# Kernel tuning notes

Measured on AMD Instinct MI355X. Metric: run time of the kernel, lower is better.

Reference implementation:

```python
import jax, jax.numpy as jnp
import numpy as np
from jax import lax

B, C, H, W = 4, 192, 64, 64
D_STATE, D_CONV, EXPAND = 16, 4, 2
D_INNER = EXPAND * C           # 384
DT_RANK = (C + 15) // 16       # 12 (mamba_ssm default ceil(d_model/16))


def setup_inputs() -> dict:
    key = jax.random.key(0)
    ks = jax.random.split(key, 12)
    sc = lambda k, shape, s=0.02: (jax.random.normal(k, shape, jnp.float32) * s)
    x = jax.random.normal(ks[0], (B, C, H, W), jnp.float32)
    norm_w = jnp.ones((C,), jnp.float32)
    norm_b = jnp.zeros((C,), jnp.float32)
    in_proj_w = sc(ks[1], (2 * D_INNER, C))
    conv_w = sc(ks[2], (D_INNER, D_CONV), 0.1)
    conv_b = jnp.zeros((D_INNER,), jnp.float32)
    x_proj_w = sc(ks[3], (DT_RANK + 2 * D_STATE, D_INNER))
    dt_proj_w = sc(ks[4], (D_INNER, DT_RANK), 0.1)
    # dt bias init so softplus(dt_bias) is in a realistic [1e-3, 1e-1] range
    dt0 = jax.random.uniform(ks[5], (D_INNER,), jnp.float32, 0.001, 0.1)
    dt_proj_b = jnp.log(jnp.expm1(dt0))
    A_log = jnp.log(jnp.broadcast_to(
        jnp.arange(1, D_STATE + 1, dtype=jnp.float32), (D_INNER, D_STATE)))
    D = jnp.ones((D_INNER,), jnp.float32)
    out_proj_w = sc(ks[6], (C, D_INNER))
    return {"x": x, "norm_w": norm_w, "norm_b": norm_b, "in_proj_w": in_proj_w,
            "conv_w": conv_w, "conv_b": conv_b, "x_proj_w": x_proj_w,
            "dt_proj_w": dt_proj_w, "dt_proj_b": dt_proj_b, "A_log": A_log,
            "D": D, "out_proj_w": out_proj_w}


def _mamba2d(x, norm_w, norm_b, in_proj_w, conv_w, conv_b, x_proj_w,
             dt_proj_w, dt_proj_b, A_log, D, out_proj_w):
    b, c, h, w = x.shape
    L = h * w
    seq = x.reshape(b, c, L).transpose(0, 2, 1)            # (B, L, C)
    # LayerNorm over channel dim
    mu = seq.mean(-1, keepdims=True)
    var = ((seq - mu) ** 2).mean(-1, keepdims=True)
    seqn = (seq - mu) * lax.rsqrt(var + 1e-5) * norm_w + norm_b
    # in_proj -> (x, z)
    xz = seqn @ in_proj_w.T                                # (B, L, 2*d_inner)
    xin, z = jnp.split(xz, 2, axis=-1)
    # causal depthwise conv1d over L
    xc = xin.transpose(0, 2, 1)                            # (B, d_inner, L)
    xc = lax.conv_general_dilated(xc, conv_w[:, None, :], (1,),
                                  [(D_CONV - 1, 0)],
                                  feature_group_count=D_INNER)
    xc = jax.nn.silu(xc + conv_b[None, :, None])
    xs = xc.transpose(0, 2, 1)                             # (B, L, d_inner)
    # input-dependent dt, B, C
    dbl = xs @ x_proj_w.T                                  # (B, L, dt_rank+2n)
    dt = dbl[..., :DT_RANK]
    Bm = dbl[..., DT_RANK:DT_RANK + D_STATE]               # (B, L, n)
    Cm = dbl[..., DT_RANK + D_STATE:]                      # (B, L, n)
    dt = jax.nn.softplus(dt @ dt_proj_w.T + dt_proj_b)     # (B, L, d_inner)
    A = -jnp.exp(A_log)                                    # (d_inner, n)
    dA = jnp.exp(dt[..., None] * A)                        # (B, L, d_inner, n)
    dBx = jnp.einsum('bld,bln->bldn', dt * xs, Bm)         # (B, L, d_inner, n)
    # selective scan over L
    def step(hcar, inp):
        dA_t, dBx_t, C_t = inp
        hcar = dA_t * hcar + dBx_t                         # (B, d_inner, n)
        y_t = jnp.einsum('bdn,bn->bd', hcar, C_t)
        return hcar, y_t
    h0 = jnp.zeros((b, D_INNER, D_STATE), xs.dtype)
    _, ys = lax.scan(step, h0, (jnp.moveaxis(dA, 1, 0),
                                jnp.moveaxis(dBx, 1, 0),
                                jnp.moveaxis(Cm, 1, 0)))
    y = jnp.moveaxis(ys, 0, 1) + xs * D                    # (B, L, d_inner)
    y = y * jax.nn.silu(z)
    out = y @ out_proj_w.T                                 # (B, L, C)
    return x + out.transpose(0, 2, 1).reshape(b, c, h, w)


def reference(x, norm_w, norm_b, in_proj_w, conv_w, conv_b, x_proj_w,
              dt_proj_w, dt_proj_b, A_log, D, out_proj_w):
    return _mamba2d(x, norm_w, norm_b, in_proj_w, conv_w, conv_b, x_proj_w,
                    dt_proj_w, dt_proj_b, A_log, D, out_proj_w)
```

## Files before the change

kernel.cpp:

```cpp
#include <hip/hip_runtime.h>
#include <hip/hip_bf16.h>

constexpr int B_ = 4;
constexpr int C_ = 192;
constexpr int L_ = 4096;
constexpr int DI = 384;
constexpr int DSs = 16;
constexpr int DTR = 12;
constexpr int NDBL = 44;
constexpr int NCHUNK = 256;
constexpr int CSZ = 16;
constexpr int NSUP = 16;

constexpr size_t BL = (size_t)B_ * L_;

constexpr size_t F_SEQN = 0;
constexpr size_t F_XIN  = F_SEQN + BL * C_ / 2;
constexpr size_t F_Z    = F_XIN + BL * DI / 2;
constexpr size_t F_XSB  = F_Z + BL * DI / 2;
constexpr size_t F_DBL  = F_XSB + BL * DI / 2;
constexpr size_t F_DT   = F_DBL + BL * NDBL;
constexpr size_t F_SBUF = F_DT + BL * DI / 2;
constexpr size_t F_HLOC = F_SBUF + (size_t)B_ * NCHUNK * DI;
constexpr size_t F_SPRE = F_HLOC + (size_t)B_ * NCHUNK * DI * 16 / 2;
constexpr size_t F_HSUP = F_SPRE + (size_t)B_ * NCHUNK * DI;
constexpr size_t F_SSUP = F_HSUP + (size_t)B_ * NSUP * 16 * DI;
constexpr size_t F_ISUP = F_SSUP + (size_t)B_ * NSUP * DI;
constexpr size_t F_WBUF = F_ISUP + (size_t)B_ * NSUP * 16 * DI;

typedef __attribute__((ext_vector_type(8))) short bf16x8;
typedef __attribute__((ext_vector_type(4))) float f32x4;

__device__ __forceinline__ unsigned short f2bf(float v) {
  unsigned x = __builtin_bit_cast(unsigned, v);
  unsigned r = x + 0x7FFFu + ((x >> 16) & 1u);
  return (unsigned short)(r >> 16);
}
__device__ __forceinline__ float bf2f(unsigned short u) {
  return __builtin_bit_cast(float, (unsigned)u << 16);
}
__device__ __forceinline__ void gload16(const void* g, void* l) {
  __builtin_amdgcn_global_load_lds((const __attribute__((address_space(1))) void*)g,
                                   (__attribute__((address_space(3))) void*)l, 16, 0, 0);
}
#define MFMA16(a, b, c) __builtin_amdgcn_mfma_f32_16x16x32_bf16(a, b, c, 0, 0, 0)

__global__ __launch_bounds__(256) void k_ln(const float* __restrict__ x,
                                            const float* __restrict__ nw,
                                            const float* __restrict__ nb,
                                            unsigned short* __restrict__ seqn,
                                            const float* __restrict__ ipw,
                                            const float* __restrict__ xpw,
                                            const float* __restrict__ opw,
                                            unsigned short* __restrict__ wbuf) {
  if (blockIdx.x >= 1024) {
    int t = (blockIdx.x - 1024) * 256 + threadIdx.x;
    if (t < 239616) {
      float v;
      if (t < 147456) v = ipw[t];
      else if (t < 165888) {
        int j = t - 147456;
        int r = j / 384, c = j - r * 384;
        v = (r < 44) ? xpw[r * 384 + c] : 0.f;
      } else v = opw[t - 165888];
      wbuf[t] = f2bf(v);
    }
    return;
  }
  __shared__ unsigned short xt[192][18];
  __shared__ float ps[16][16], ps2[16][16];
  __shared__ float mu_[16], rs_[16];
  __shared__ float wsh[192], bsh[192];
  int tid = threadIdx.x;
  int blk = blockIdx.x;
  int b = blk >> 8;
  int l0 = (blk & 255) << 4;
  const float* xb = x + (size_t)b * C_ * L_;
  for (int idx = tid; idx < 192 * 4; idx += 256) {
    int c = idx >> 2, lq = idx & 3;
    float4 v = *(const float4*)&xb[(size_t)c * L_ + l0 + (lq << 2)];
    ushort2 u0, u1;
    u0.x = f2bf(v.x); u0.y = f2bf(v.y);
    u1.x = f2bf(v.z); u1.y = f2bf(v.w);
    *(ushort2*)&xt[c][(lq << 2)] = u0;
    *(ushort2*)&xt[c][(lq << 2) + 2] = u1;
  }
  if (tid < 192) { wsh[tid] = nw[tid]; bsh[tid] = nb[tid]; }
  __syncthreads();
  int ll = tid & 15, q = tid >> 4;
  float s = 0.f, ss = 0.f;
  for (int c = q * 12; c < q * 12 + 12; ++c) {
    float v = bf2f(xt[c][ll]);
    s += v; ss += v * v;
  }
  ps[q][ll] = s; ps2[q][ll] = ss;
  __syncthreads();
  if (q == 0) {
    float st = 0.f, sst = 0.f;
#pragma unroll
    for (int g = 0; g < 16; ++g) { st += ps[g][ll]; sst += ps2[g][ll]; }
    float mu = st * (1.f / 192.f);
    float var = sst * (1.f / 192.f) - mu * mu;
    mu_[ll] = mu; rs_[ll] = rsqrtf(var + 1e-5f);
  }
  __syncthreads();
  unsigned short* so = seqn + ((size_t)b * L_ + l0) * C_;
  for (int idx = tid; idx < 16 * 192; idx += 256) {
    int l = idx / 192, c = idx - l * 192;
    so[idx] = f2bf((bf2f(xt[c][l]) - mu_[l]) * rs_[l] * wsh[c] + bsh[c]);
  }
}

__global__ __launch_bounds__(256) void k_inproj(const unsigned short* __restrict__ A,
                                                const unsigned short* __restrict__ W,
                                                unsigned short* __restrict__ xin,
                                                unsigned short* __restrict__ z) {
  __shared__ unsigned short smem[16384];
  unsigned short* As = smem;
  unsigned short* Bs = smem + 8192;
  int tid = threadIdx.x;
  int w = tid >> 6, l = tid & 63;
  int wr = w >> 1, wc = w & 1;
  int m0 = blockIdx.x << 7;
  int n0 = blockIdx.y << 7;
  f32x4 acc[4][4];
#pragma unroll
  for (int i = 0; i < 4; ++i)
#pragma unroll
    for (int j = 0; j < 4; ++j) acc[i][j] = (f32x4){0.f, 0.f, 0.f, 0.f};
  int lr = l & 15, lk = l >> 4;
  for (int kt = 0; kt < 3; ++kt) {
    int k0 = kt * 64;
    if (kt) __syncthreads();
#pragma unroll
    for (int i = 0; i < 4; ++i) {
      int row = (i << 5) + (tid >> 3);
      int gc = k0 + (((tid & 7) ^ (row & 7)) << 3);
      gload16(A + (size_t)(m0 + row) * 192 + gc, &As[(i << 11) + (w << 9)]);
      gload16(W + (size_t)(n0 + row) * 192 + gc, &Bs[(i << 11) + (w << 9)]);
    }
    __syncthreads();
#pragma unroll
    for (int ks = 0; ks < 2; ++ks) {
      int s = (ks << 2) + lk;
      bf16x8 af[4], bfr[4];
#pragma unroll
      for (int mi = 0; mi < 4; ++mi) {
        int r = (wr << 6) + (mi << 4) + lr;
        af[mi] = *(const bf16x8*)&As[r * 64 + ((s ^ (r & 7)) << 3)];
      }
#pragma unroll
      for (int ni = 0; ni < 4; ++ni) {
        int r = (wc << 6) + (ni << 4) + lr;
        bfr[ni] = *(const bf16x8*)&Bs[r * 64 + ((s ^ (r & 7)) << 3)];
      }
#pragma unroll
      for (int mi = 0; mi < 4; ++mi)
#pragma unroll
        for (int ni = 0; ni < 4; ++ni) acc[mi][ni] = MFMA16(af[mi], bfr[ni], acc[mi][ni]);
    }
  }
  __syncthreads();
#pragma unroll
  for (int mi = 0; mi < 4; ++mi)
#pragma unroll
    for (int ni = 0; ni < 4; ++ni) {
      int col = (wc << 6) + (ni << 4) + lr;
#pragma unroll
      for (int r = 0; r < 4; ++r) {
        int row = (wr << 6) + (mi << 4) + (lk << 2) + r;
        smem[(row << 7) + col] = f2bf(acc[mi][ni][r]);
      }
    }
  __syncthreads();
#pragma unroll
  for (int i = 0; i < 8; ++i) {
    int chunk = i * 256 + tid;
    int row = chunk >> 4, cq = chunk & 15;
    int n = n0 + (cq << 3);
    unsigned short* dst = (n < 384) ? (xin + (size_t)(m0 + row) * DI + n)
                                    : (z + (size_t)(m0 + row) * DI + (n - 384));
    *(bf16x8*)dst = *(const bf16x8*)&smem[(row << 7) + (cq << 3)];
  }
}

__global__ __launch_bounds__(384) void k_convx(const unsigned short* __restrict__ xin,
                                               const float* __restrict__ cw,
                                               const float* __restrict__ cb,
                                               const unsigned short* __restrict__ W,
                                               unsigned short* __restrict__ xsb,
                                               float* __restrict__ dbl) {
  __shared__ unsigned short xs[6 * 2048];
  __shared__ unsigned short Bs[3072];
  int tid = threadIdx.x;
  int w = tid >> 6, l = tid & 63;
  int b = blockIdx.y;
  int l0 = blockIdx.x << 5;
  int d = tid;
  float4 w4 = *(const float4*)&cw[d * 4];
  float bb = cb[d];
  const unsigned short* xp = xin + ((size_t)b * L_ + l0) * DI + d;
  unsigned short* op = xsb + ((size_t)b * L_ + l0) * DI + d;
  float x0 = 0.f, x1 = 0.f, x2 = 0.f;
  if (l0 > 0) {
    x0 = bf2f(*(xp - 3 * DI));
    x1 = bf2f(*(xp - 2 * DI));
    x2 = bf2f(*(xp - DI));
  }
  int kt = d >> 6, col = d & 63, g = col >> 3, e = col & 7;
  unsigned short* xsrow = xs + kt * 2048;
  for (int r = 0; r < 32; ++r) {
    float xv = bf2f(xp[(size_t)r * DI]);
    float a = bb + w4.x * x0 + w4.y * x1 + w4.z * x2 + w4.w * xv;
    float sv = a * __builtin_amdgcn_rcpf(1.f + __expf(-a));
    unsigned short sb = f2bf(sv);
    xsrow[r * 64 + ((g ^ (r & 7)) << 3) + e] = sb;
    op[(size_t)r * DI] = sb;
    x0 = x1; x1 = x2; x2 = xv;
  }
  __syncthreads();
  int lr = l & 15, lk = l >> 4;
  f32x4 acc[3];
#pragma unroll
  for (int i = 0; i < 3; ++i) acc[i] = (f32x4){0.f, 0.f, 0.f, 0.f};
  for (int kt2 = 0; kt2 < 6; ++kt2) {
    int k0 = kt2 * 64;
    if (kt2) __syncthreads();
    {
      int row = tid >> 3;
      int gc = k0 + (((tid & 7) ^ (row & 7)) << 3);
      gload16(W + (size_t)row * 384 + gc, &Bs[w << 9]);
    }
    __syncthreads();
    if (w < 2) {
#pragma unroll
      for (int ks = 0; ks < 2; ++ks) {
        int s = (ks << 2) + lk;
        int ar = (w << 4) + lr;
        bf16x8 a = *(const bf16x8*)&xs[kt2 * 2048 + ar * 64 + ((s ^ (ar & 7)) << 3)];
#pragma unroll
        for (int ni = 0; ni < 3; ++ni) {
          int br = (ni << 4) + lr;
          bf16x8 bbv = *(const bf16x8*)&Bs[br * 64 + ((s ^ (br & 7)) << 3)];
          acc[ni] = MFMA16(a, bbv, acc[ni]);
        }
      }
    }
  }
  if (w < 2) {
#pragma unroll
    for (int ni = 0; ni < 3; ++ni)
#pragma unroll
      for (int r = 0; r < 4; ++r) {
        int colq = (ni << 4) + lr;
        if (colq < NDBL)
          dbl[((size_t)b * L_ + l0 + (w << 4) + (lk << 2) + r) * NDBL + colq] = acc[ni][r];
      }
  }
}

__global__ __launch_bounds__(384) void k_scanA(const unsigned short* __restrict__ xsb,
                                               const float* __restrict__ dbl,
                                               const float* __restrict__ dw,
                                               const float* __restrict__ dbias,
                                               const float* __restrict__ A_log,
                                               unsigned short* __restrict__ dtb,
                                               unsigned short* __restrict__ Hloc,
                                               float* __restrict__ Sbuf) {
  __shared__ float Bsh[CSZ][16];
  __shared__ float dl[CSZ][12];
  int tid = threadIdx.x;
  int blk = blockIdx.x;
  int b = blk >> 8;
  int chunk = blk & (NCHUNK - 1);
  int l0 = chunk * CSZ;
  for (int idx = tid; idx < CSZ * 28; idx += 384) {
    int r = idx / 28, c = idx - r * 28;
    float v = dbl[((size_t)b * L_ + l0 + r) * NDBL + c];
    if (c < 12) dl[r][c] = v; else Bsh[r][c - 12] = v;
  }
  int d = tid;
  float4 wv0 = *(const float4*)&dw[d * 12];
  float4 wv1 = *(const float4*)&dw[d * 12 + 4];
  float4 wv2 = *(const float4*)&dw[d * 12 + 8];
  float bias = dbias[d];
  bool fast = true;
#pragma unroll
  for (int n = 0; n < 16; ++n) {
    float An_ = -__expf(A_log[d * 16 + n]);
    fast = fast && (fabsf(An_ + (float)(n + 1)) < 2e-3f);
  }
  const unsigned short* xp = xsb + ((size_t)b * L_ + l0) * DI + d;
  unsigned short* dtp = dtb + ((size_t)b * L_ + l0) * DI + d;
  __syncthreads();
  float h[16];
#pragma unroll
  for (int n = 0; n < 16; ++n) h[n] = 0.f;
  float S = 0.f;
  if (fast) {
#pragma unroll
    for (int i = 0; i < CSZ; ++i) {
      float4 c0 = *(const float4*)&dl[i][0];
      float4 c1 = *(const float4*)&dl[i][4];
      float4 c2 = *(const float4*)&dl[i][8];
      float a = bias;
      a = fmaf(wv0.x, c0.x, a); a = fmaf(wv0.y, c0.y, a);
      a = fmaf(wv0.z, c0.z, a); a = fmaf(wv0.w, c0.w, a);
      a = fmaf(wv1.x, c1.x, a); a = fmaf(wv1.y, c1.y, a);
      a = fmaf(wv1.z, c1.z, a); a = fmaf(wv1.w, c1.w, a);
      a = fmaf(wv2.x, c2.x, a); a = fmaf(wv2.y, c2.y, a);
      a = fmaf(wv2.z, c2.z, a); a = fmaf(wv2.w, c2.w, a);
      float sp = fmaxf(a, 0.f) + __logf(1.f + __expf(-fabsf(a)));
      dtp[(size_t)i * DI] = f2bf(sp);
      S += sp;
      float xv = bf2f(xp[(size_t)i * DI]);
      float dtx = sp * xv;
      float r = __expf(-sp);
      float r2 = r * r;
      float r4 = r2 * r2;
      float dA0 = r, dA1 = r2, dA2 = r2 * r, dA3 = r4;
#pragma unroll
      for (int g = 0; g < 4; ++g) {
        float4 Bg = *(const float4*)&Bsh[i][g << 2];
        h[(g << 2) + 0] = fmaf(dA0, h[(g << 2) + 0], dtx * Bg.x);
        h[(g << 2) + 1] = fmaf(dA1, h[(g << 2) + 1], dtx * Bg.y);
        h[(g << 2) + 2] = fmaf(dA2, h[(g << 2) + 2], dtx * Bg.z);
        h[(g << 2) + 3] = fmaf(dA3, h[(g << 2) + 3], dtx * Bg.w);
        if (g < 3) { dA0 *= r4; dA1 *= r4; dA2 *= r4; dA3 *= r4; }
      }
    }
  } else {
    float An[16];
#pragma unroll
    for (int n = 0; n < 16; ++n) An[n] = -__expf(A_log[d * 16 + n]);
#pragma unroll
    for (int i = 0; i < CSZ; ++i) {
      float4 c0 = *(const float4*)&dl[i][0];
      float4 c1 = *(const float4*)&dl[i][4];
      float4 c2 = *(const float4*)&dl[i][8];
      float a = bias;
      a = fmaf(wv0.x, c0.x, a); a = fmaf(wv0.y, c0.y, a);
      a = fmaf(wv0.z, c0.z, a); a = fmaf(wv0.w, c0.w, a);
      a = fmaf(wv1.x, c1.x, a); a = fmaf(wv1.y, c1.y, a);
      a = fmaf(wv1.z, c1.z, a); a = fmaf(wv1.w, c1.w, a);
      a = fmaf(wv2.x, c2.x, a); a = fmaf(wv2.y, c2.y, a);
      a = fmaf(wv2.z, c2.z, a); a = fmaf(wv2.w, c2.w, a);
      float sp = fmaxf(a, 0.f) + __logf(1.f + __expf(-fabsf(a)));
      dtp[(size_t)i * DI] = f2bf(sp);
      S += sp;
      float xv = bf2f(xp[(size_t)i * DI]);
      float dtx = sp * xv;
#pragma unroll
      for (int n = 0; n < 16; ++n)
        h[n] = fmaf(__expf(sp * An[n]), h[n], dtx * Bsh[i][n]);
    }
  }
  size_t hbase = ((size_t)(b * NCHUNK + chunk) * 16) * DI + d;
#pragma unroll
  for (int n = 0; n < 16; ++n) Hloc[hbase + (size_t)n * DI] = f2bf(h[n]);
  Sbuf[((size_t)b * NCHUNK + chunk) * DI + d] = S;
}

__global__ __launch_bounds__(384) void k_scanB1(const float* __restrict__ A_log,
                                                unsigned short* __restrict__ Hloc,
                                                const float* __restrict__ Sbuf,
                                                float* __restrict__ Spre,
                                                float* __restrict__ Hsup,
                                                float* __restrict__ Ssup) {
  int d = threadIdx.x;
  int blk = blockIdx.x;
  int n = blk & 15;
  int s = (blk >> 4) & 15;
  int b = blk >> 8;
  float An = -__expf(A_log[d * 16 + n]);
  float h = 0.f, Sp = 0.f;
  int c0 = s * 16;
#pragma unroll
  for (int i = 0; i < 16; ++i) {
    int c = c0 + i;
    size_t hidx = (((size_t)(b * NCHUNK + c) * 16) + n) * DI + d;
    float Hl = bf2f(Hloc[hidx]);
    float S = Sbuf[((size_t)b * NCHUNK + c) * DI + d];
    Hloc[hidx] = f2bf(h);
    if (n == 0) Spre[((size_t)b * NCHUNK + c) * DI + d] = Sp;
    h = fmaf(__expf(An * S), h, Hl);
    Sp += S;
  }
  Hsup[(((size_t)(b * NSUP + s) * 16) + n) * DI + d] = h;
  if (n == 0) Ssup[((size_t)b * NSUP + s) * DI + d] = Sp;
}

__global__ __launch_bounds__(384) void k_scanB2(const float* __restrict__ A_log,
                                                const float* __restrict__ Hsup,
                                                const float* __restrict__ Ssup,
                                                float* __restrict__ Isup) {
  int d = threadIdx.x;
  int blk = blockIdx.x;
  int n = blk & 15;
  int b = blk >> 4;
  float An = -__expf(A_log[d * 16 + n]);
  float I = 0.f;
#pragma unroll
  for (int s = 0; s < NSUP; ++s) {
    size_t idx = (((size_t)(b * NSUP + s) * 16) + n) * DI + d;
    Isup[idx] = I;
    I = fmaf(__expf(An * Ssup[((size_t)b * NSUP + s) * DI + d]), I, Hsup[idx]);
  }
}

__global__ __launch_bounds__(384) void k_scanC(const unsigned short* __restrict__ xsb,
                                               const unsigned short* __restrict__ dtb,
                                               const float* __restrict__ dbl,
                                               const unsigned short* __restrict__ z,
                                               const float* __restrict__ A_log,
                                               const float* __restrict__ Dw,
                                               const unsigned short* __restrict__ Hloc,
                                               const float* __restrict__ Spre,
                                               const float* __restrict__ Isup,
                                               const unsigned short* __restrict__ Wo,
                                               const float* __restrict__ x,
                                               float* __restrict__ out) {
  __shared__ float BCsh[CSZ][32];
  __shared__ unsigned short yt[6 * 1024];
  __shared__ unsigned short Bs[12288];
  int tid = threadIdx.x;
  int blk = blockIdx.x;
  int b = blk >> 8;
  int chunk = blk & (NCHUNK - 1);
  int l0 = chunk * CSZ;
  for (int idx = tid; idx < CSZ * 32; idx += 384) {
    int r = idx >> 5, n32 = idx & 31;
    BCsh[r][n32] = dbl[((size_t)b * L_ + l0 + r) * NDBL + DTR + n32];
  }
  int d = tid;
  float Dd = Dw[d];
  bool fast = true;
#pragma unroll
  for (int n = 0; n < 16; ++n) {
    float An_ = -__expf(A_log[d * 16 + n]);
    fast = fast && (fabsf(An_ + (float)(n + 1)) < 2e-3f);
  }
  int sup = chunk >> 4;
  size_t hbase = ((size_t)(b * NCHUNK + chunk) * 16) * DI + d;
  size_t ibase = ((size_t)(b * NSUP + sup) * 16) * DI + d;
  float Spv = Spre[((size_t)b * NCHUNK + chunk) * DI + d];
  float h[16];
  if (fast) {
    float t = __expf(-Spv);
    float t2 = t * t;
    float t4 = t2 * t2;
    float p0 = t, p1 = t2, p2 = t2 * t, p3 = t4;
#pragma unroll
    for (int g = 0; g < 4; ++g) {
      h[(g << 2) + 0] = fmaf(p0, Isup[ibase + (size_t)((g << 2) + 0) * DI],
                             bf2f(Hloc[hbase + (size_t)((g << 2) + 0) * DI]));
      h[(g << 2) + 1] = fmaf(p1, Isup[ibase + (size_t)((g << 2) + 1) * DI],
                             bf2f(Hloc[hbase + (size_t)((g << 2) + 1) * DI]));
      h[(g << 2) + 2] = fmaf(p2, Isup[ibase + (size_t)((g << 2) + 2) * DI],
                             bf2f(Hloc[hbase + (size_t)((g << 2) + 2) * DI]));
      h[(g << 2) + 3] = fmaf(p3, Isup[ibase + (size_t)((g << 2) + 3) * DI],
                             bf2f(Hloc[hbase + (size_t)((g << 2) + 3) * DI]));
      if (g < 3) { p0 *= t4; p1 *= t4; p2 *= t4; p3 *= t4; }
    }
  } else {
#pragma unroll
    for (int n = 0; n < 16; ++n) {
      float An_ = -__expf(A_log[d * 16 + n]);
      h[n] = fmaf(__expf(An_ * Spv), Isup[ibase + (size_t)n * DI],
                  bf2f(Hloc[hbase + (size_t)n * DI]));
    }
  }
  const unsigned short* xp = xsb + ((size_t)b * L_ + l0) * DI + d;
  const unsigned short* dtp = dtb + ((size_t)b * L_ + l0) * DI + d;
  const unsigned short* zp = z + ((size_t)b * L_ + l0) * DI + d;
  int ktile = d >> 6, colq = d & 63, gq = colq >> 3, eq = colq & 7;
  unsigned short* ytp = yt + ktile * 1024;
  __syncthreads();
  if (fast) {
#pragma unroll
    for (int i = 0; i < CSZ; ++i) {
      float sp = bf2f(dtp[(size_t)i * DI]);
      float xv = bf2f(xp[(size_t)i * DI]);
      float zv = bf2f(zp[(size_t)i * DI]);
      float dtx = sp * xv;
      float r = __expf(-sp);
      float r2 = r * r;
      float r4 = r2 * r2;
      float dA0 = r, dA1 = r2, dA2 = r2 * r, dA3 = r4;
      float y = 0.f;
#pragma unroll
      for (int g = 0; g < 4; ++g) {
        float4 Bg = *(const float4*)&BCsh[i][g << 2];
        float4 Cg = *(const float4*)&BCsh[i][16 + (g << 2)];
        h[(g << 2) + 0] = fmaf(dA0, h[(g << 2) + 0], dtx * Bg.x);
        h[(g << 2) + 1] = fmaf(dA1, h[(g << 2) + 1], dtx * Bg.y);
        h[(g << 2) + 2] = fmaf(dA2, h[(g << 2) + 2], dtx * Bg.z);
        h[(g << 2) + 3] = fmaf(dA3, h[(g << 2) + 3], dtx * Bg.w);
        y = fmaf(h[(g << 2) + 0], Cg.x, y);
        y = fmaf(h[(g << 2) + 1], Cg.y, y);
        y = fmaf(h[(g << 2) + 2], Cg.z, y);
        y = fmaf(h[(g << 2) + 3], Cg.w, y);
        if (g < 3) { dA0 *= r4; dA1 *= r4; dA2 *= r4; dA3 *= r4; }
      }
      y = fmaf(xv, Dd, y);
      float sig = __builtin_amdgcn_rcpf(1.f + __expf(-zv));
      ytp[i * 64 + ((gq ^ (i & 7)) << 3) + eq] = f2bf(y * (zv * sig));
    }
  } else {
    float An[16];
#pragma unroll
    for (int n = 0; n < 16; ++n) An[n] = -__expf(A_log[d * 16 + n]);
#pragma unroll
    for (int i = 0; i < CSZ; ++i) {
      float sp = bf2f(dtp[(size_t)i * DI]);
      float xv = bf2f(xp[(size_t)i * DI]);
      float zv = bf2f(zp[(size_t)i * DI]);
      float dtx = sp * xv;
      float y = 0.f;
#pragma unroll
      for (int n = 0; n < 16; ++n) {
        h[n] = fmaf(__expf(sp * An[n]), h[n], dtx * BCsh[i][n]);
        y = fmaf(h[n], BCsh[i][16 + n], y);
      }
      y = fmaf(xv, Dd, y);
      float sig = __builtin_amdgcn_rcpf(1.f + __expf(-zv));
      ytp[i * 64 + ((gq ^ (i & 7)) << 3) + eq] = f2bf(y * (zv * sig));
    }
  }
  int w = tid >> 6, l = tid & 63;
  int lr = l & 15, lk = l >> 4;
  f32x4 acc[2];
  acc[0] = (f32x4){0.f, 0.f, 0.f, 0.f};
  acc[1] = (f32x4){0.f, 0.f, 0.f, 0.f};
  for (int kt = 0; kt < 6; ++kt) {
    int k0 = kt * 64;
    __syncthreads();
#pragma unroll
    for (int j = 0; j < 4; ++j) {
      int row = j * 48 + (tid >> 3);
      int gc = k0 + (((tid & 7) ^ (row & 7)) << 3);
      gload16(Wo + (size_t)row * 384 + gc, &Bs[j * 3072 + (w << 9)]);
    }
    __syncthreads();
#pragma unroll
    for (int ks = 0; ks < 2; ++ks) {
      int s = (ks << 2) + lk;
      bf16x8 a = *(const bf16x8*)&yt[kt * 1024 + lr * 64 + ((s ^ (lr & 7)) << 3)];
#pragma unroll
      for (int ni = 0; ni < 2; ++ni) {
        int br = ((w << 1) + ni) * 16 + lr;
        bf16x8 bv = *(const bf16x8*)&Bs[br * 64 + ((s ^ (br & 7)) << 3)];
        acc[ni] = MFMA16(a, bv, acc[ni]);
      }
    }
  }
#pragma unroll
  for (int ni = 0; ni < 2; ++ni) {
    int c = ((w << 1) + ni) * 16 + lr;
    size_t off = ((size_t)b * C_ + c) * L_ + l0 + (lk << 2);
    f32x4 xv = *(const f32x4*)&x[off];
    *(f32x4*)&out[off] = acc[ni] + xv;
  }
}

extern "C" void kernel_launch(void* const* d_in, const int* in_sizes, int n_in,
                              void* d_out, int out_size, void* d_ws, size_t ws_size,
                              hipStream_t stream) {
  const float* x         = (const float*)d_in[0];
  const float* norm_w    = (const float*)d_in[1];
  const float* norm_b    = (const float*)d_in[2];
  const float* in_proj_w = (const float*)d_in[3];
  const float* conv_w    = (const float*)d_in[4];
  const float* conv_b    = (const float*)d_in[5];
  const float* x_proj_w  = (const float*)d_in[6];
  const float* dt_proj_w = (const float*)d_in[7];
  const float* dt_proj_b = (const float*)d_in[8];
  const float* A_log     = (const float*)d_in[9];
  const float* Dw        = (const float*)d_in[10];
  const float* out_proj_w= (const float*)d_in[11];
  float* out = (float*)d_out;
  float* ws = (float*)d_ws;

  unsigned short* seqn = (unsigned short*)(ws + F_SEQN);
  unsigned short* xin  = (unsigned short*)(ws + F_XIN);
  unsigned short* z    = (unsigned short*)(ws + F_Z);
  unsigned short* xsb  = (unsigned short*)(ws + F_XSB);
  float* dbl           = ws + F_DBL;
  unsigned short* dtb  = (unsigned short*)(ws + F_DT);
  float* Sbuf          = ws + F_SBUF;
  unsigned short* Hloc = (unsigned short*)(ws + F_HLOC);
  float* Spre          = ws + F_SPRE;
  float* Hsup          = ws + F_HSUP;
  float* Ssup          = ws + F_SSUP;
  float* Isup          = ws + F_ISUP;
  unsigned short* wbuf = (unsigned short*)(ws + F_WBUF);
  unsigned short* ipw  = wbuf;
  unsigned short* xpw  = wbuf + 147456;
  unsigned short* opw  = wbuf + 165888;

  hipLaunchKernelGGL(k_ln, dim3(1960), dim3(256), 0, stream, x, norm_w, norm_b, seqn,
                     in_proj_w, x_proj_w, out_proj_w, wbuf);
  hipLaunchKernelGGL(k_inproj, dim3(128, 6), dim3(256), 0, stream, seqn, ipw, xin, z);
  hipLaunchKernelGGL(k_convx, dim3(128, 4), dim3(384), 0, stream, xin, conv_w, conv_b, xpw, xsb,
                     dbl);
  hipLaunchKernelGGL(k_scanA, dim3(1024), dim3(384), 0, stream, xsb, dbl, dt_proj_w, dt_proj_b,
                     A_log, dtb, Hloc, Sbuf);
  hipLaunchKernelGGL(k_scanB1, dim3(1024), dim3(384), 0, stream, A_log, Hloc, Sbuf, Spre, Hsup,
                     Ssup);
  hipLaunchKernelGGL(k_scanB2, dim3(64), dim3(384), 0, stream, A_log, Hsup, Ssup, Isup);
  hipLaunchKernelGGL(k_scanC, dim3(1024), dim3(384), 0, stream, xsb, dtb, dbl, z, A_log, Dw,
                     Hloc, Spre, Isup, opw, x, out);
}
```

Before: 106.2 us.

## Fuse chunk scan pass into conv/x_proj kernel and double scan chunk size

The first chunked-scan pass is merged into the conv+x_proj kernel. It reuses the 32-row tile already held in shared memory (conv output and the dt/B projections) instead of re-reading them from global memory in a separate launch. Scan chunks grow from 16 to 32 rows so the chunk grid matches the conv tiling. The later scan kernels and the output-projection MFMA tiling are adjusted to 32-row tiles. This removes one launch and a global round trip, but halves the block count for the scan kernels and lengthens the serial per-chunk work.

New measurement: 97.23 us. -8.4%, faster.

```diff
diff --git a/kernel.cpp b/kernel.cpp
--- a/kernel.cpp
+++ b/kernel.cpp
@@ -8,9 +8,9 @@
 constexpr int DSs = 16;
 constexpr int DTR = 12;
 constexpr int NDBL = 44;
-constexpr int NCHUNK = 256;
-constexpr int CSZ = 16;
-constexpr int NSUP = 16;
+constexpr int NCHUNK = 128;
+constexpr int CSZ = 32;
+constexpr int NSUP = 8;
 
 constexpr size_t BL = (size_t)B_ * L_;
 
@@ -188,14 +188,23 @@
                                                const float* __restrict__ cw,
                                                const float* __restrict__ cb,
                                                const unsigned short* __restrict__ W,
+                                               const float* __restrict__ dw,
+                                               const float* __restrict__ dbias,
+                                               const float* __restrict__ A_log,
                                                unsigned short* __restrict__ xsb,
-                                               float* __restrict__ dbl) {
+                                               float* __restrict__ dbl,
+                                               unsigned short* __restrict__ dtb,
+                                               unsigned short* __restrict__ Hloc,
+                                               float* __restrict__ Sbuf) {
   __shared__ unsigned short xs[6 * 2048];
   __shared__ unsigned short Bs[3072];
+  __shared__ float dl[CSZ][12];
+  __shared__ float Bsh2[CSZ][16];
   int tid = threadIdx.x;
   int w = tid >> 6, l = tid & 63;
   int b = blockIdx.y;
-  int l0 = blockIdx.x << 5;
+  int chunk = blockIdx.x;
+  int l0 = chunk << 5;
   int d = tid;
   float4 w4 = *(const float4*)&cw[d * 4];
   float bb = cb[d];
@@ -253,33 +262,14 @@
 #pragma unroll
       for (int r = 0; r < 4; ++r) {
         int colq = (ni << 4) + lr;
-        if (colq < NDBL)
-          dbl[((size_t)b * L_ + l0 + (w << 4) + (lk << 2) + r) * NDBL + colq] = acc[ni][r];
-      }
-  }
-}
-
-__global__ __launch_bounds__(384) void k_scanA(const unsigned short* __restrict__ xsb,
-                                               const float* __restrict__ dbl,
-                                               const float* __restrict__ dw,
-                                               const float* __restrict__ dbias,
-                                               const float* __restrict__ A_log,
-                                               unsigned short* __restrict__ dtb,
-                                               unsigned short* __restrict__ Hloc,
-                                               float* __restrict__ Sbuf) {
-  __shared__ float Bsh[CSZ][16];
-  __shared__ float dl[CSZ][12];
-  int tid = threadIdx.x;
-  int blk = blockIdx.x;
-  int b = blk >> 8;
-  int chunk = blk & (NCHUNK - 1);
-  int l0 = chunk * CSZ;
-  for (int idx = tid; idx < CSZ * 28; idx += 384) {
-    int r = idx / 28, c = idx - r * 28;
-    float v = dbl[((size_t)b * L_ + l0 + r) * NDBL + c];
-    if (c < 12) dl[r][c] = v; else Bsh[r][c - 12] = v;
-  }
-  int d = tid;
+        int row = (w << 4) + (lk << 2) + r;
+        float v = acc[ni][r];
+        if (colq < NDBL) dbl[((size_t)b * L_ + l0 + row) * NDBL + colq] = v;
+        if (colq < 12) dl[row][colq] = v;
+        else if (colq < 28) Bsh2[row][colq - 12] = v;
+      }
+  }
+  __syncthreads();
   float4 wv0 = *(const float4*)&dw[d * 12];
   float4 wv1 = *(const float4*)&dw[d * 12 + 4];
   float4 wv2 = *(const float4*)&dw[d * 12 + 8];
@@ -290,9 +280,7 @@
     float An_ = -__expf(A_log[d * 16 + n]);
     fast = fast && (fabsf(An_ + (float)(n + 1)) < 2e-3f);
   }
-  const unsigned short* xp = xsb + ((size_t)b * L_ + l0) * DI + d;
   unsigned short* dtp = dtb + ((size_t)b * L_ + l0) * DI + d;
-  __syncthreads();
   float h[16];
 #pragma unroll
   for (int n = 0; n < 16; ++n) h[n] = 0.f;
@@ -313,20 +301,20 @@
       float sp = fmaxf(a, 0.f) + __logf(1.f + __expf(-fabsf(a)));
       dtp[(size_t)i * DI] = f2bf(sp);
       S += sp;
-      float xv = bf2f(xp[(size_t)i * DI]);
+      float xv = bf2f(xsrow[i * 64 + ((g ^ (i & 7)) << 3) + e]);
       float dtx = sp * xv;
       float r = __expf(-sp);
       float r2 = r * r;
       float r4 = r2 * r2;
       float dA0 = r, dA1 = r2, dA2 = r2 * r, dA3 = r4;
 #pragma unroll
-      for (int g = 0; g < 4; ++g) {
-        float4 Bg = *(const float4*)&Bsh[i][g << 2];
-        h[(g << 2) + 0] = fmaf(dA0, h[(g << 2) + 0], dtx * Bg.x);
-        h[(g << 2) + 1] = fmaf(dA1, h[(g << 2) + 1], dtx * Bg.y);
-        h[(g << 2) + 2] = fmaf(dA2, h[(g << 2) + 2], dtx * Bg.z);
-        h[(g << 2) + 3] = fmaf(dA3, h[(g << 2) + 3], dtx * Bg.w);
-        if (g < 3) { dA0 *= r4; dA1 *= r4; dA2 *= r4; dA3 *= r4; }
+      for (int gg = 0; gg < 4; ++gg) {
+        float4 Bg = *(const float4*)&Bsh2[i][gg << 2];
+        h[(gg << 2) + 0] = fmaf(dA0, h[(gg << 2) + 0], dtx * Bg.x);
+        h[(gg << 2) + 1] = fmaf(dA1, h[(gg << 2) + 1], dtx * Bg.y);
+        h[(gg << 2) + 2] = fmaf(dA2, h[(gg << 2) + 2], dtx * Bg.z);
+        h[(gg << 2) + 3] = fmaf(dA3, h[(gg << 2) + 3], dtx * Bg.w);
+        if (gg < 3) { dA0 *= r4; dA1 *= r4; dA2 *= r4; dA3 *= r4; }
       }
     }
   } else {
@@ -348,11 +336,11 @@
       float sp = fmaxf(a, 0.f) + __logf(1.f + __expf(-fabsf(a)));
       dtp[(size_t)i * DI] = f2bf(sp);
       S += sp;
-      float xv = bf2f(xp[(size_t)i * DI]);
+      float xv = bf2f(xsrow[i * 64 + ((g ^ (i & 7)) << 3) + e]);
       float dtx = sp * xv;
 #pragma unroll
       for (int n = 0; n < 16; ++n)
-        h[n] = fmaf(__expf(sp * An[n]), h[n], dtx * Bsh[i][n]);
+        h[n] = fmaf(__expf(sp * An[n]), h[n], dtx * Bsh2[i][n]);
     }
   }
   size_t hbase = ((size_t)(b * NCHUNK + chunk) * 16) * DI + d;
@@ -370,8 +358,8 @@
   int d = threadIdx.x;
   int blk = blockIdx.x;
   int n = blk & 15;
-  int s = (blk >> 4) & 15;
-  int b = blk >> 8;
+  int s = (blk >> 4) & 7;
+  int b = blk >> 7;
   float An = -__expf(A_log[d * 16 + n]);
   float h = 0.f, Sp = 0.f;
   int c0 = s * 16;
@@ -421,13 +409,13 @@
                                                const float* __restrict__ x,
                                                float* __restrict__ out) {
   __shared__ float BCsh[CSZ][32];
-  __shared__ unsigned short yt[6 * 1024];
+  __shared__ unsigned short yt[6 * 2048];
   __shared__ unsigned short Bs[12288];
   int tid = threadIdx.x;
   int blk = blockIdx.x;
-  int b = blk >> 8;
+  int b = blk >> 7;
   int chunk = blk & (NCHUNK - 1);
-  int l0 = chunk * CSZ;
+  int l0 = chunk << 5;
   for (int idx = tid; idx < CSZ * 32; idx += 384) {
     int r = idx >> 5, n32 = idx & 31;
     BCsh[r][n32] = dbl[((size_t)b * L_ + l0 + r) * NDBL + DTR + n32];
@@ -474,7 +462,7 @@
   const unsigned short* dtp = dtb + ((size_t)b * L_ + l0) * DI + d;
   const unsigned short* zp = z + ((size_t)b * L_ + l0) * DI + d;
   int ktile = d >> 6, colq = d & 63, gq = colq >> 3, eq = colq & 7;
-  unsigned short* ytp = yt + ktile * 1024;
+  unsigned short* ytp = yt + ktile * 2048;
   __syncthreads();
   if (fast) {
 #pragma unroll
@@ -529,9 +517,11 @@
   }
   int w = tid >> 6, l = tid & 63;
   int lr = l & 15, lk = l >> 4;
-  f32x4 acc[2];
-  acc[0] = (f32x4){0.f, 0.f, 0.f, 0.f};
-  acc[1] = (f32x4){0.f, 0.f, 0.f, 0.f};
+  int mt = w & 1;
+  int ng = w >> 1;
+  f32x4 acc[4];
+#pragma unroll
+  for (int j = 0; j < 4; ++j) acc[j] = (f32x4){0.f, 0.f, 0.f, 0.f};
   for (int kt = 0; kt < 6; ++kt) {
     int k0 = kt * 64;
     __syncthreads();
@@ -545,21 +535,21 @@
 #pragma unroll
     for (int ks = 0; ks < 2; ++ks) {
       int s = (ks << 2) + lk;
-      bf16x8 a = *(const bf16x8*)&yt[kt * 1024 + lr * 64 + ((s ^ (lr & 7)) << 3)];
-#pragma unroll
-      for (int ni = 0; ni < 2; ++ni) {
-        int br = ((w << 1) + ni) * 16 + lr;
+      bf16x8 a = *(const bf16x8*)&yt[kt * 2048 + (mt * 16 + lr) * 64 + ((s ^ (lr & 7)) << 3)];
+#pragma unroll
+      for (int j = 0; j < 4; ++j) {
+        int br = (ng * 4 + j) * 16 + lr;
         bf16x8 bv = *(const bf16x8*)&Bs[br * 64 + ((s ^ (br & 7)) << 3)];
-        acc[ni] = MFMA16(a, bv, acc[ni]);
-      }
-    }
-  }
-#pragma unroll
-  for (int ni = 0; ni < 2; ++ni) {
-    int c = ((w << 1) + ni) * 16 + lr;
-    size_t off = ((size_t)b * C_ + c) * L_ + l0 + (lk << 2);
+        acc[j] = MFMA16(a, bv, acc[j]);
+      }
+    }
+  }
+#pragma unroll
+  for (int j = 0; j < 4; ++j) {
+    int c = (ng * 4 + j) * 16 + lr;
+    size_t off = ((size_t)b * C_ + c) * L_ + l0 + mt * 16 + (lk << 2);
     f32x4 xv = *(const f32x4*)&x[off];
-    *(f32x4*)&out[off] = acc[ni] + xv;
+    *(f32x4*)&out[off] = acc[j] + xv;
   }
 }
 
@@ -601,13 +591,11 @@
   hipLaunchKernelGGL(k_ln, dim3(1960), dim3(256), 0, stream, x, norm_w, norm_b, seqn,
                      in_proj_w, x_proj_w, out_proj_w, wbuf);
   hipLaunchKernelGGL(k_inproj, dim3(128, 6), dim3(256), 0, stream, seqn, ipw, xin, z);
-  hipLaunchKernelGGL(k_convx, dim3(128, 4), dim3(384), 0, stream, xin, conv_w, conv_b, xpw, xsb,
-                     dbl);
-  hipLaunchKernelGGL(k_scanA, dim3(1024), dim3(384), 0, stream, xsb, dbl, dt_proj_w, dt_proj_b,
-                     A_log, dtb, Hloc, Sbuf);
-  hipLaunchKernelGGL(k_scanB1, dim3(1024), dim3(384), 0, stream, A_log, Hloc, Sbuf, Spre, Hsup,
+  hipLaunchKernelGGL(k_convx, dim3(128, 4), dim3(384), 0, stream, xin, conv_w, conv_b, xpw,
+                     dt_proj_w, dt_proj_b, A_log, xsb, dbl, dtb, Hloc, Sbuf);
+  hipLaunchKernelGGL(k_scanB1, dim3(512), dim3(384), 0, stream, A_log, Hloc, Sbuf, Spre, Hsup,
                      Ssup);
   hipLaunchKernelGGL(k_scanB2, dim3(64), dim3(384), 0, stream, A_log, Hsup, Ssup, Isup);
-  hipLaunchKernelGGL(k_scanC, dim3(1024), dim3(384), 0, stream, xsb, dtb, dbl, z, A_log, Dw,
+  hipLaunchKernelGGL(k_scanC, dim3(512), dim3(384), 0, stream, xsb, dtb, dbl, z, A_log, Dw,
                      Hloc, Spre, Isup, opw, x, out);
 }
```
